# Performance work log

Measured on AMD Instinct MI355X. Metric: run time of the kernel, lower is better.

## Reference

```python
import jax, jax.numpy as jnp
import numpy as np

H = W = 256
FX = FY = 1.0
CX = CY = 0.5


def setup_inputs() -> dict:
    key = jax.random.key(0)
    k1, k2, k3 = jax.random.split(key, 3)
    B, N = 8, 500000
    points = jax.random.normal(k1, (B, N, 3), dtype=jnp.float32)
    densities = jax.random.uniform(k2, (B, N, 1), dtype=jnp.float32)
    depth = jax.random.uniform(k3, (B, 1, H, W), dtype=jnp.float32)
    return {"points": points, "densities": densities, "depth": depth}


def project_points_to_depth(points, densities):
    # points: [B,N,3], densities: [B,N,1] -> depth grid [B,1,H,W]
    B, N, _ = points.shape
    x = points[:, :, 0]
    y = points[:, :, 1]
    z = points[:, :, 2]
    # pinhole projection; .long() in torch truncates toward zero, as does astype(int32)
    u = jnp.clip(((FX * x / z + CX) * W).astype(jnp.int32), 0, W - 1)  # [B,N]
    v = jnp.clip(((FY * y / z + CY) * H).astype(jnp.int32), 0, H - 1)  # [B,N]
    d = densities[:, :, 0]
    val = jnp.where(d > 0.5, z * d, jnp.float32(0.0))  # conditional contribution
    idx = v * W + u  # flat pixel index [B,N]
    flat = jnp.zeros((B, H * W), dtype=points.dtype)
    flat = flat.at[jnp.arange(B)[:, None], idx].add(val)  # batched scatter-add
    return flat.reshape(B, 1, H, W)


def reference(points, densities, depth):
    projected = project_points_to_depth(points, densities)
    mask = projected > 0
    diff2 = jnp.where(mask, (projected - depth) ** 2, jnp.float32(0.0))
    count = jnp.maximum(jnp.sum(mask), 1)
    # F.mse_loss over masked elements == mean of squared diffs where mask
    return jnp.sum(diff2) / count.astype(diff2.dtype)
```

## Files before the change

### kernel.cpp

```cpp
#include <hip/hip_runtime.h>

#define HH 256
#define WW 256
#define HWSZ (HH * WW)

#define CHUNK_GROUPS 512
#define NSLOTS 1022

__global__ __launch_bounds__(256, 8) void scatter_k(
    const float* __restrict__ pts, const float* __restrict__ dens,
    float* __restrict__ flat, int N)
{
    __shared__ float lds[NSLOTS];
    for (int s = threadIdx.x; s < NSLOTS; s += 256) lds[s] = 0.0f;
    __syncthreads();

    int b = blockIdx.y;
    const float* pb = pts + (size_t)b * N * 3;
    const float* db = dens + (size_t)b * N;
    float* out = flat + (size_t)b * HWSZ;

    int ngroups = N >> 2;
    int gbase = blockIdx.x * CHUNK_GROUPS;
    const float4* p4 = (const float4*)pb;
    const float4* d4 = (const float4*)db;

    float corner[4] = {0.0f, 0.0f, 0.0f, 0.0f};

    int g0 = gbase + threadIdx.x;
    int g1 = g0 + 256;
    bool ok0 = g0 < ngroups;
    bool ok1 = g1 < ngroups;
    int gc0 = ok0 ? g0 : (ngroups - 1);
    int gc1 = ok1 ? g1 : (ngroups - 1);

    float4 a0 = p4[3 * gc0], b0 = p4[3 * gc0 + 1], c0 = p4[3 * gc0 + 2];
    float4 a1 = p4[3 * gc1], b1 = p4[3 * gc1 + 1], c1 = p4[3 * gc1 + 2];
    float4 d0 = d4[gc0];
    float4 d1 = d4[gc1];
    if (!ok0) { d0.x = d0.y = d0.z = d0.w = 0.0f; }
    if (!ok1) { d1.x = d1.y = d1.z = d1.w = 0.0f; }

    auto proc = [&](const float4& a, const float4& bb, const float4& c,
                    const float4& dd) {
        float xs[4] = {a.x, a.w, bb.z, c.y};
        float ys[4] = {a.y, bb.x, bb.w, c.z};
        float zs[4] = {a.z, bb.y, c.x, c.w};
        float ds[4] = {dd.x, dd.y, dd.z, dd.w};

        #pragma unroll
        for (int k = 0; k < 4; k++) {
            float d = ds[k];
            float z = zs[k];
            bool acc = d > 0.5f;
            float r = 256.0f / z;
            float uf = fmaf(xs[k], r, 128.0f);
            float vf = fmaf(ys[k], r, 128.0f);
            int u = (int)fminf(fmaxf(uf, 0.0f), 255.0f);
            int v = (int)fminf(fmaxf(vf, 0.0f), 255.0f);
            float val = z * d;

            bool u0 = (u == 0), u255 = (u == 255);
            bool v0 = (v == 0), v255 = (v == 255);
            bool ub = u0 | u255;
            bool vb = v0 | v255;
            bool iscorner = acc & ub & vb;
            bool isborder = acc & (ub ^ vb);
            bool isinter  = acc & !ub & !vb;

            int ci = (v255 ? 2 : 0) | (u255 ? 1 : 0);
            corner[0] += (iscorner && ci == 0) ? val : 0.0f;
            corner[1] += (iscorner && ci == 1) ? val : 0.0f;
            corner[2] += (iscorner && ci == 2) ? val : 0.0f;
            corner[3] += (iscorner && ci == 3) ? val : 0.0f;

            int slot = v0 ? u : (v255 ? 256 + u : (u0 ? 511 + v : 767 + v));
            if (isborder) atomicAdd(&lds[slot], val);
            if (isinter)  atomicAdd(out + v * WW + u, val);
        }
    };

    proc(a0, b0, c0, d0);
    proc(a1, b1, c1, d1);

    #pragma unroll
    for (int j = 0; j < 4; j++) {
        float v = corner[j];
        #pragma unroll
        for (int off = 32; off > 0; off >>= 1) v += __shfl_down(v, off);
        if ((threadIdx.x & 63) == 0) {
            const int cslot[4] = {0, 255, 256, 511};
            atomicAdd(&lds[cslot[j]], v);
        }
    }

    __syncthreads();
    for (int s = threadIdx.x; s < NSLOTS; s += 256) {
        float v = lds[s];
        if (v != 0.0f) {
            int u, vv;
            if (s < 256)      { vv = 0;        u = s; }
            else if (s < 512) { vv = 255;      u = s - 256; }
            else if (s < 768) { u = 0;         vv = s - 512 + 1; }
            else              { u = 255;       vv = s - 768 + 1; }
            atomicAdd(out + vv * WW + u, v);
        }
    }
}

#define LBLOCKS 128
#define ELEMS_PER_THREAD 4
__global__ __launch_bounds__(256) void loss_k(
    const float* __restrict__ flat, const float* __restrict__ depth,
    float* __restrict__ accum, int* __restrict__ done,
    float* __restrict__ out, int total4, int nblocks)
{
    const float4* f4 = (const float4*)flat;
    const float4* z4 = (const float4*)depth;

    int i0 = blockIdx.x * blockDim.x + threadIdx.x;
    int stride = gridDim.x * blockDim.x;

    float4 p[ELEMS_PER_THREAD], q[ELEMS_PER_THREAD];
    bool ok[ELEMS_PER_THREAD];
    #pragma unroll
    for (int k = 0; k < ELEMS_PER_THREAD; k++) {
        int i = i0 + k * stride;
        ok[k] = i < total4;
        if (ok[k]) { p[k] = f4[i]; q[k] = z4[i]; }
    }
    float s = 0.0f;
    int c = 0;
    for (int i = i0 + ELEMS_PER_THREAD * stride; i < total4; i += stride) {
        float4 pp = f4[i];
        float4 qq = z4[i];
        if (pp.x > 0.0f) { float df = pp.x - qq.x; s += df * df; c++; }
        if (pp.y > 0.0f) { float df = pp.y - qq.y; s += df * df; c++; }
        if (pp.z > 0.0f) { float df = pp.z - qq.z; s += df * df; c++; }
        if (pp.w > 0.0f) { float df = pp.w - qq.w; s += df * df; c++; }
    }
    #pragma unroll
    for (int k = 0; k < ELEMS_PER_THREAD; k++) {
        if (ok[k]) {
            float4 pp = p[k], qq = q[k];
            if (pp.x > 0.0f) { float df = pp.x - qq.x; s += df * df; c++; }
            if (pp.y > 0.0f) { float df = pp.y - qq.y; s += df * df; c++; }
            if (pp.z > 0.0f) { float df = pp.z - qq.z; s += df * df; c++; }
            if (pp.w > 0.0f) { float df = pp.w - qq.w; s += df * df; c++; }
        }
    }

    #pragma unroll
    for (int off = 32; off > 0; off >>= 1) {
        s += __shfl_down(s, off);
        c += __shfl_down(c, off);
    }

    __shared__ float bsum[4];
    __shared__ int bcnt[4];
    int wave = threadIdx.x >> 6;
    if ((threadIdx.x & 63) == 0) { bsum[wave] = s; bcnt[wave] = c; }
    __syncthreads();
    if (threadIdx.x == 0) {
        float ts = bsum[0] + bsum[1] + bsum[2] + bsum[3];
        int tc = bcnt[0] + bcnt[1] + bcnt[2] + bcnt[3];
        atomicAdd(accum, ts);
        atomicAdd((int*)accum + 1, tc);
        __threadfence();
        int old = atomicAdd(done, 1);
        if (old == nblocks - 1) {
            float fs = atomicAdd(accum, 0.0f);
            int fc = atomicAdd((int*)accum + 1, 0);
            out[0] = fs / (float)(fc >= 1 ? fc : 1);
        }
    }
}

extern "C" void kernel_launch(void* const* d_in, const int* in_sizes, int n_in,
                              void* d_out, int out_size, void* d_ws, size_t ws_size,
                              hipStream_t stream) {
    const float* pts   = (const float*)d_in[0];
    const float* dens  = (const float*)d_in[1];
    const float* depth = (const float*)d_in[2];
    float* out = (float*)d_out;

    int B = in_sizes[2] / HWSZ;
    int N = in_sizes[0] / (3 * B);

    float* flat  = (float*)d_ws;
    float* accum = flat + (size_t)B * HWSZ;
    int*   done  = (int*)(accum + 16);

    hipMemsetAsync(d_ws, 0, ((size_t)B * HWSZ + 32) * sizeof(float), stream);

    int ngroups = N / 4;
    int cblocks = (ngroups + CHUNK_GROUPS - 1) / CHUNK_GROUPS;
    dim3 sgrid(cblocks, B);
    scatter_k<<<sgrid, 256, 0, stream>>>(pts, dens, flat, N);

    int total4 = B * HWSZ / 4;
    loss_k<<<dim3(LBLOCKS), 256, 0, stream>>>(flat, depth, accum, done, out,
                                              total4, LBLOCKS);
}
```

Baseline: 132.3 us.

## Use persistent grid-stride scatter blocks with software-prefetched loads and fast reciprocal

The scatter kernel changes from many small blocks, each handling two groups per thread, to a fixed grid of 128 blocks per batch. Each thread loops over its chunk and prefetches the next group's point and density loads while processing the current one. This amortizes the per-block LDS zeroing, border flush and corner reductions over more points and overlaps memory latency with compute. The division is replaced by the hardware reciprocal, which can differ slightly from the reference at pixel boundaries, and launch bounds drop to 4 blocks per CU.

```diff
diff --git a/kernel.cpp b/kernel.cpp
--- a/kernel.cpp
+++ b/kernel.cpp
@@ -4,10 +4,10 @@
 #define WW 256
 #define HWSZ (HH * WW)
 
-#define CHUNK_GROUPS 512
+#define GRIDX 128
 #define NSLOTS 1022
 
-__global__ __launch_bounds__(256, 8) void scatter_k(
+__global__ __launch_bounds__(256, 4) void scatter_k(
     const float* __restrict__ pts, const float* __restrict__ dens,
     float* __restrict__ flat, int N)
 {
@@ -21,25 +21,15 @@
     float* out = flat + (size_t)b * HWSZ;
 
     int ngroups = N >> 2;
-    int gbase = blockIdx.x * CHUNK_GROUPS;
+    int gpb = (ngroups + GRIDX - 1) / GRIDX;
+    int gbase = blockIdx.x * gpb;
+    int gend = min(gbase + gpb, ngroups);
+    int nit = (gpb + 255) >> 8;
+    int last = ngroups - 1;
     const float4* p4 = (const float4*)pb;
     const float4* d4 = (const float4*)db;
 
     float corner[4] = {0.0f, 0.0f, 0.0f, 0.0f};
-
-    int g0 = gbase + threadIdx.x;
-    int g1 = g0 + 256;
-    bool ok0 = g0 < ngroups;
-    bool ok1 = g1 < ngroups;
-    int gc0 = ok0 ? g0 : (ngroups - 1);
-    int gc1 = ok1 ? g1 : (ngroups - 1);
-
-    float4 a0 = p4[3 * gc0], b0 = p4[3 * gc0 + 1], c0 = p4[3 * gc0 + 2];
-    float4 a1 = p4[3 * gc1], b1 = p4[3 * gc1 + 1], c1 = p4[3 * gc1 + 2];
-    float4 d0 = d4[gc0];
-    float4 d1 = d4[gc1];
-    if (!ok0) { d0.x = d0.y = d0.z = d0.w = 0.0f; }
-    if (!ok1) { d1.x = d1.y = d1.z = d1.w = 0.0f; }
 
     auto proc = [&](const float4& a, const float4& bb, const float4& c,
                     const float4& dd) {
@@ -53,7 +43,7 @@
             float d = ds[k];
             float z = zs[k];
             bool acc = d > 0.5f;
-            float r = 256.0f / z;
+            float r = __builtin_amdgcn_rcpf(z) * 256.0f;
             float uf = fmaf(xs[k], r, 128.0f);
             float vf = fmaf(ys[k], r, 128.0f);
             int u = (int)fminf(fmaxf(uf, 0.0f), 255.0f);
@@ -80,8 +70,28 @@
         }
     };
 
-    proc(a0, b0, c0, d0);
-    proc(a1, b1, c1, d1);
+    int g = gbase + threadIdx.x;
+    int gc = min(g, last);
+    float4 A  = p4[3 * gc];
+    float4 Bv = p4[3 * gc + 1];
+    float4 C  = p4[3 * gc + 2];
+    float4 D  = d4[gc];
+    if (g >= gend) { D.x = D.y = D.z = D.w = 0.0f; }
+
+    for (int it = 0; it < nit; ++it) {
+        int gn = g + 256;
+        int gnc = min(gn, last);
+        float4 nA  = p4[3 * gnc];
+        float4 nB  = p4[3 * gnc + 1];
+        float4 nC  = p4[3 * gnc + 2];
+        float4 nD  = d4[gnc];
+        if (gn >= gend) { nD.x = nD.y = nD.z = nD.w = 0.0f; }
+
+        proc(A, Bv, C, D);
+
+        A = nA; Bv = nB; C = nC; D = nD;
+        g = gn;
+    }
 
     #pragma unroll
     for (int j = 0; j < 4; j++) {
@@ -193,9 +203,7 @@
 
     hipMemsetAsync(d_ws, 0, ((size_t)B * HWSZ + 32) * sizeof(float), stream);
 
-    int ngroups = N / 4;
-    int cblocks = (ngroups + CHUNK_GROUPS - 1) / CHUNK_GROUPS;
-    dim3 sgrid(cblocks, B);
+    dim3 sgrid(GRIDX, B);
     scatter_k<<<sgrid, 256, 0, stream>>>(pts, dens, flat, N);
 
     int total4 = B * HWSZ / 4;
```

After: 122.9 us. 7.2% less time.
